# Performance work log

Hardware: AMD Instinct MI355X
Metric: run time of the kernel (lower is better)

The kernel has to match this reference:

```python
import jax, jax.numpy as jnp
import numpy as np


def setup_inputs() -> dict:
    key = jax.random.key(0)
    k1, k2, k3 = jax.random.split(key, 3)
    B, D, C = 16384, 1024, 14
    z_image = jax.random.normal(k1, (B, D), dtype=jnp.float32)
    z_text = jax.random.normal(k2, (B, D), dtype=jnp.float32)
    labels = jax.random.randint(k3, (B, C), 0, 2, dtype=jnp.int32)
    return {"z_image": z_image, "z_text": z_text, "labels": labels}


def _margins(labels):
    # labels: [B, C] binary; imposter index j = (i+1) % B -> roll by -1
    lj = jnp.roll(labels, -1, axis=0)
    equal = jnp.all(labels == lj, axis=1)                     # [B]
    n = jnp.sum(labels | lj, axis=1).astype(jnp.float32)      # union size
    d = jnp.sum(labels ^ lj, axis=1).astype(jnp.float32)      # hamming diff
    m = jnp.where(n > 0, jnp.maximum(0.5, d / jnp.maximum(n, 1.0)), 0.5)
    return jnp.where(equal, 0.0, m)                           # [B]


def reference(z_image, z_text, labels):
    # similarity_function == 'dot' (default path of the torch module)
    margin = _margins(labels)                                  # [B]
    paired = jnp.sum(z_image * z_text, axis=1)                 # dot(img_i, txt_i)
    imp_img = jnp.sum(jnp.roll(z_image, -1, axis=0) * z_text, axis=1)  # dot(img_j, txt_i)
    imp_txt = jnp.sum(jnp.roll(z_text, -1, axis=0) * z_image, axis=1)  # dot(txt_j, img_i)
    loss_img = jnp.mean(jax.nn.relu(imp_img - paired + margin))
    loss_txt = jnp.mean(jax.nn.relu(imp_txt - paired + margin))
    return loss_img + loss_txt
```

## Files before the change

### kernel.cpp

```cpp
#include <hip/hip_runtime.h>


constexpr int D   = 1024;
constexpr int C   = 14;
constexpr int RPW = 4;
constexpr int WPB = 4;
constexpr int RPB = RPW * WPB;

__device__ __forceinline__ float dot4(const float4 x, const float4 y) {
    return x.x * y.x + x.y * y.y + x.z * y.z + x.w * y.w;
}

__global__ __launch_bounds__(256) void rank_phase1(
    const float* __restrict__ zi, const float* __restrict__ zt,
    const int* __restrict__ labels, float* __restrict__ partial, int B)
{
    const int wave = threadIdx.x >> 6;
    const int lane = threadIdx.x & 63;
    const int r0   = blockIdx.x * RPB + wave * RPW;
    const int M    = B - 1;

    const float4* zi_r[RPW + 1];
    const float4* zt_r[RPW + 1];
    #pragma unroll
    for (int k = 0; k <= RPW; ++k) {
        const int r = (r0 + k) & M;
        zi_r[k] = (const float4*)(zi + (size_t)r * D);
        zt_r[k] = (const float4*)(zt + (size_t)r * D);
    }

    float p [RPW] = {0.f, 0.f, 0.f, 0.f};
    float ii[RPW] = {0.f, 0.f, 0.f, 0.f};
    float it[RPW] = {0.f, 0.f, 0.f, 0.f};

    #pragma unroll
    for (int j = 0; j < 4; ++j) {
        const int idx = lane + 64 * j;
        float4 a[RPW + 1], b[RPW + 1];
        #pragma unroll
        for (int k = 0; k <= RPW; ++k) a[k] = zi_r[k][idx];
        #pragma unroll
        for (int k = 0; k <= RPW; ++k) b[k] = zt_r[k][idx];
        #pragma unroll
        for (int k = 0; k < RPW; ++k) {
            p [k] += dot4(a[k],     b[k]);
            ii[k] += dot4(a[k + 1], b[k]);
            it[k] += dot4(b[k + 1], a[k]);
        }
    }

    const int kk = lane >> 4;
    const int c  = lane & 15;
    int lx = 0, lo = 0;
    if (c < C) {
        const int ra = (r0 + kk)     & M;
        const int rb = (r0 + kk + 1) & M;
        const int li = labels[(size_t)ra * C + c];
        const int lj = labels[(size_t)rb * C + c];
        lx = li ^ lj;
        lo = li | lj;
    }
    const unsigned long long bx = __ballot(lx != 0);
    const unsigned long long bo = __ballot(lo != 0);

    #pragma unroll
    for (int off = 32; off > 0; off >>= 1) {
        #pragma unroll
        for (int k = 0; k < RPW; ++k) {
            p [k] += __shfl_down(p [k], off, 64);
            ii[k] += __shfl_down(ii[k], off, 64);
            it[k] += __shfl_down(it[k], off, 64);
        }
    }

    float local = 0.f;
    if (lane == 0) {
        #pragma unroll
        for (int k = 0; k < RPW; ++k) {
            const float dv = (float)__popcll((bx >> (16 * k)) & 0x3FFFull);
            const float nv = (float)__popcll((bo >> (16 * k)) & 0x3FFFull);
            const float m  = (dv == 0.f) ? 0.f : fmaxf(0.5f, dv / nv);
            local += fmaxf(ii[k] - p[k] + m, 0.f)
                   + fmaxf(it[k] - p[k] + m, 0.f);
        }
    }

    __shared__ float smem[WPB];
    if (lane == 0) smem[wave] = local;
    __syncthreads();
    if (threadIdx.x == 0)
        partial[blockIdx.x] = smem[0] + smem[1] + smem[2] + smem[3];
}

__global__ __launch_bounds__(256) void rank_phase2(
    const float* __restrict__ partial, float* __restrict__ out,
    int npart, float invB)
{
    float s = 0.f;
    for (int i = threadIdx.x; i < npart; i += 256) s += partial[i];
    #pragma unroll
    for (int off = 32; off > 0; off >>= 1) s += __shfl_down(s, off, 64);
    __shared__ float sm[4];
    if ((threadIdx.x & 63) == 0) sm[threadIdx.x >> 6] = s;
    __syncthreads();
    if (threadIdx.x == 0)
        out[0] = (sm[0] + sm[1] + sm[2] + sm[3]) * invB;
}

extern "C" void kernel_launch(void* const* d_in, const int* in_sizes, int n_in,
                              void* d_out, int out_size, void* d_ws, size_t ws_size,
                              hipStream_t stream) {
    const float* zi     = (const float*)d_in[0];
    const float* zt     = (const float*)d_in[1];
    const int*   labels = (const int*)d_in[2];
    float*       out    = (float*)d_out;
    float*       ws     = (float*)d_ws;

    const int B      = in_sizes[0] / D;
    const int blocks = B / RPB;

    rank_phase1<<<blocks, 256, 0, stream>>>(zi, zt, labels, ws, B);
    rank_phase2<<<1, 256, 0, stream>>>(ws, out, blocks, 1.0f / (float)B);
}
```

Before: 150.4 us.

## Split each row's dot products across all four waves of a block and swizzle blocks

Each block now handles 4 rows instead of 16. The 1024-element dimension is split across the four waves, each reading one float4 per row, rather than each wave looping over the full row. The 12 partial dots are combined through shared memory, and block IDs are remapped in groups of 8, likely to spread neighbouring rows across XCDs or channels. This gives four times as many blocks, which may improve memory-level parallelism. The cost is more shuffle work per useful byte, an extra shared-memory reduction, and a larger partial array for phase 2 to sum.

```diff
diff --git a/kernel.cpp b/kernel.cpp
--- a/kernel.cpp
+++ b/kernel.cpp
@@ -3,9 +3,8 @@
 
 constexpr int D   = 1024;
 constexpr int C   = 14;
-constexpr int RPW = 4;
+constexpr int RPB = 4;
 constexpr int WPB = 4;
-constexpr int RPB = RPW * WPB;
 
 __device__ __forceinline__ float dot4(const float4 x, const float4 y) {
     return x.x * y.x + x.y * y.y + x.z * y.z + x.w * y.w;
@@ -17,79 +16,75 @@
 {
     const int wave = threadIdx.x >> 6;
     const int lane = threadIdx.x & 63;
-    const int r0   = blockIdx.x * RPB + wave * RPW;
-    const int M    = B - 1;
 
-    const float4* zi_r[RPW + 1];
-    const float4* zt_r[RPW + 1];
-    #pragma unroll
-    for (int k = 0; k <= RPW; ++k) {
-        const int r = (r0 + k) & M;
-        zi_r[k] = (const float4*)(zi + (size_t)r * D);
-        zt_r[k] = (const float4*)(zt + (size_t)r * D);
-    }
+    const int nwg = gridDim.x;
+    const int wg  = (blockIdx.x & 7) * (nwg >> 3) + (blockIdx.x >> 3);
 
-    float p [RPW] = {0.f, 0.f, 0.f, 0.f};
-    float ii[RPW] = {0.f, 0.f, 0.f, 0.f};
-    float it[RPW] = {0.f, 0.f, 0.f, 0.f};
+    const int r0 = wg * RPB;
+    const int M  = B - 1;
 
-    #pragma unroll
-    for (int j = 0; j < 4; ++j) {
-        const int idx = lane + 64 * j;
-        float4 a[RPW + 1], b[RPW + 1];
-        #pragma unroll
-        for (int k = 0; k <= RPW; ++k) a[k] = zi_r[k][idx];
-        #pragma unroll
-        for (int k = 0; k <= RPW; ++k) b[k] = zt_r[k][idx];
-        #pragma unroll
-        for (int k = 0; k < RPW; ++k) {
-            p [k] += dot4(a[k],     b[k]);
-            ii[k] += dot4(a[k + 1], b[k]);
-            it[k] += dot4(b[k + 1], a[k]);
+    const int idx = (wave << 6) + lane;
+
+    int lx = 0, lo = 0;
+    {
+        const int kk = lane >> 4, c = lane & 15;
+        if (wave == 0 && c < C) {
+            const int ra = (r0 + kk)     & M;
+            const int rb = (r0 + kk + 1) & M;
+            const int li = labels[(size_t)ra * C + c];
+            const int lj = labels[(size_t)rb * C + c];
+            lx = li ^ lj;
+            lo = li | lj;
         }
     }
 
-    const int kk = lane >> 4;
-    const int c  = lane & 15;
-    int lx = 0, lo = 0;
-    if (c < C) {
-        const int ra = (r0 + kk)     & M;
-        const int rb = (r0 + kk + 1) & M;
-        const int li = labels[(size_t)ra * C + c];
-        const int lj = labels[(size_t)rb * C + c];
-        lx = li ^ lj;
-        lo = li | lj;
+    float4 a[RPB + 1], b[RPB + 1];
+    #pragma unroll
+    for (int k = 0; k <= RPB; ++k) {
+        const int r = (r0 + k) & M;
+        a[k] = ((const float4*)(zi + (size_t)r * D))[idx];
+        b[k] = ((const float4*)(zt + (size_t)r * D))[idx];
     }
-    const unsigned long long bx = __ballot(lx != 0);
-    const unsigned long long bo = __ballot(lo != 0);
+
+    float v[12];
+    #pragma unroll
+    for (int k = 0; k < RPB; ++k) {
+        v[k]     = dot4(a[k],     b[k]);
+        v[4 + k] = dot4(a[k + 1], b[k]);
+        v[8 + k] = dot4(b[k + 1], a[k]);
+    }
 
     #pragma unroll
     for (int off = 32; off > 0; off >>= 1) {
         #pragma unroll
-        for (int k = 0; k < RPW; ++k) {
-            p [k] += __shfl_down(p [k], off, 64);
-            ii[k] += __shfl_down(ii[k], off, 64);
-            it[k] += __shfl_down(it[k], off, 64);
+        for (int i = 0; i < 12; ++i) v[i] += __shfl_down(v[i], off, 64);
+    }
+
+    __shared__ float red[WPB][12];
+    if (lane == 0) {
+        #pragma unroll
+        for (int i = 0; i < 12; ++i) red[wave][i] = v[i];
+    }
+    __syncthreads();
+
+    if (wave == 0) {
+        const unsigned long long bx = __ballot(lx != 0);
+        const unsigned long long bo = __ballot(lo != 0);
+        if (lane == 0) {
+            float local = 0.f;
+            #pragma unroll
+            for (int k = 0; k < RPB; ++k) {
+                const float p  = red[0][k]     + red[1][k]     + red[2][k]     + red[3][k];
+                const float di = red[0][4 + k] + red[1][4 + k] + red[2][4 + k] + red[3][4 + k];
+                const float dt = red[0][8 + k] + red[1][8 + k] + red[2][8 + k] + red[3][8 + k];
+                const float dv = (float)__popcll((bx >> (16 * k)) & 0x3FFFull);
+                const float nv = (float)__popcll((bo >> (16 * k)) & 0x3FFFull);
+                const float m  = (dv == 0.f) ? 0.f : fmaxf(0.5f, dv / nv);
+                local += fmaxf(di - p + m, 0.f) + fmaxf(dt - p + m, 0.f);
+            }
+            partial[wg] = local;
         }
     }
-
-    float local = 0.f;
-    if (lane == 0) {
-        #pragma unroll
-        for (int k = 0; k < RPW; ++k) {
-            const float dv = (float)__popcll((bx >> (16 * k)) & 0x3FFFull);
-            const float nv = (float)__popcll((bo >> (16 * k)) & 0x3FFFull);
-            const float m  = (dv == 0.f) ? 0.f : fmaxf(0.5f, dv / nv);
-            local += fmaxf(ii[k] - p[k] + m, 0.f)
-                   + fmaxf(it[k] - p[k] + m, 0.f);
-        }
-    }
-
-    __shared__ float smem[WPB];
-    if (lane == 0) smem[wave] = local;
-    __syncthreads();
-    if (threadIdx.x == 0)
-        partial[blockIdx.x] = smem[0] + smem[1] + smem[2] + smem[3];
 }
 
 __global__ __launch_bounds__(256) void rank_phase2(
```

Result: slower. 161.6 us (+7.4%).
